# Performance work log

Hardware: AMD Instinct MI355X
Metric: run time of the kernel (lower is better)

The kernel has to match this reference:

```python
import jax, jax.numpy as jnp
import numpy as np

K = 3  # Chebyshev filter size (max_view)


def avwgcn(X, E, weights_pool, bias_pool):
    """Adaptive node-wise graph conv. X: [B,N,C_in], E: [N,D]."""
    N = E.shape[0]
    # adaptive adjacency: softmax over rows of relu(E E^T)
    supports = jax.nn.softmax(jax.nn.relu(E @ E.T), axis=1)  # [N,N]
    support_set = [jnp.eye(N, dtype=X.dtype), supports]
    for _ in range(2, K):  # Chebyshev recursion
        support_set.append(2.0 * supports @ support_set[-1] - support_set[-2])
    S = jnp.stack(support_set, axis=0)  # [K,N,N]
    W = jnp.einsum('nd,dkio->nkio', E, weights_pool)  # per-node weights [N,K,Ci,Co]
    bias = E @ bias_pool  # [N,Co]
    XG = jnp.einsum('knm,bmc->bnkc', S, X)  # [B,N,K,Ci]
    return jnp.einsum('bnki,nkio->bno', XG, W) + bias  # [B,N,Co]


def setup_inputs() -> dict:
    key = jax.random.key(0)
    ks = jax.random.split(key, 5)
    B, N, Cin, Cout, D = 32, 4096, 2, 64, 10
    Ci = Cin + Cout  # 66
    X = jax.random.normal(ks[0], (B, N, Cin), dtype=jnp.float32)
    H = jnp.zeros((B, N, Cout), dtype=jnp.float32)
    E = jax.random.normal(ks[1], (N, D), dtype=jnp.float32)
    W_gate = jax.random.normal(ks[2], (D, K, Ci, 2 * Cout), dtype=jnp.float32) * 0.1
    b_gate = jnp.zeros((D, 2 * Cout), dtype=jnp.float32)
    W_update = jax.random.normal(ks[3], (D, K, Ci, Cout), dtype=jnp.float32) * 0.1
    b_update = jnp.zeros((D, Cout), dtype=jnp.float32)
    return {"X": X, "H": H, "E": E, "W_gate": W_gate, "b_gate": b_gate,
            "W_update": W_update, "b_update": b_update}


def reference(X, H, E, W_gate, b_gate, W_update, b_update):
    Cout = H.shape[-1]
    XH = jnp.concatenate([X, H], axis=-1)  # [B,N,Cin+Cout]
    ZR = jax.nn.sigmoid(avwgcn(XH, E, W_gate, b_gate))  # [B,N,2*Cout]
    Z, R = ZR[..., :Cout], ZR[..., Cout:]
    C = jnp.concatenate([X, Z * H], axis=-1)
    HC = jnp.tanh(avwgcn(C, E, W_update, b_update))
    return R * H + (1.0 - R) * HC
```

## Files before the change

kernel.cpp:

```cpp
#include <hip/hip_runtime.h>
#include <math.h>

#define N_NODES 4096
#define BATCH   32
#define D_EMB   10
#define CIN     2
#define COUT    64
#define CI      66
#define KSUP    3
#define NCOLS   2112
#define NPAD    2176
#define LDT     4096

#define KSEC    72
#define KI_REAL 216
#define KILD    232
#define OCH     (32 * KILD)
#define WROW_G  (128 * KILD)
#define WROW_U  (64 * KILD)
#define WGT2_R  (WROW_G + WROW_U)

typedef _Float16 half_t;
typedef __attribute__((ext_vector_type(8))) _Float16 f16x8;
typedef __attribute__((ext_vector_type(4))) _Float16 f16x4;
typedef __attribute__((ext_vector_type(2))) _Float16 f16x2;
typedef __attribute__((ext_vector_type(4))) float f32x4;

union u32h2 { unsigned u; f16x2 h; };

struct __attribute__((packed, aligned(4))) uint4_u4 { uint4 v; };
__device__ __forceinline__ f16x8 loadu8h(const half_t* p) {
  union { uint4 u; f16x8 h; } r;
  r.u = ((const uint4_u4*)p)->v;
  return r.h;
}

__device__ __forceinline__ float fast_sigmoid(float x) { return 1.f / (1.f + __expf(-x)); }
__device__ __forceinline__ float fast_tanh(float x) { return 1.f - 2.f / (__expf(2.f * x) + 1.f); }

__device__ __forceinline__ void gld_lds16(const half_t* g, half_t* l) {
  __builtin_amdgcn_global_load_lds(
      (const __attribute__((address_space(1))) void*)g,
      (__attribute__((address_space(3))) void*)l, 16, 0, 0);
}

__global__ __launch_bounds__(256) void k_softmax_p(const float* __restrict__ E,
                                                   half_t* __restrict__ Pb) {
  const int n = blockIdx.x;
  const int tid = threadIdx.x;
  __shared__ float En[D_EMB];
  __shared__ float ms[256], ss[256];
  if (tid < D_EMB) En[tid] = E[n * D_EMB + tid];
  __syncthreads();
  float en[D_EMB];
#pragma unroll
  for (int d = 0; d < D_EMB; ++d) en[d] = En[d];

  float m = -1e30f, s = 0.f;
  for (int c = tid; c < N_NODES; c += 256) {
    const float* Ec = E + c * D_EMB;
    float v = 0.f;
#pragma unroll
    for (int d = 0; d < D_EMB; ++d) v += en[d] * Ec[d];
    v = fmaxf(v, 0.f);
    if (v > m) { s *= __expf(m - v); m = v; }
    s += __expf(v - m);
  }
  ms[tid] = m; ss[tid] = s;
  __syncthreads();
  for (int off = 128; off > 0; off >>= 1) {
    if (tid < off) {
      float m2 = ms[tid + off], s2 = ss[tid + off];
      float m1 = ms[tid], s1 = ss[tid];
      float mm = fmaxf(m1, m2);
      ms[tid] = mm;
      ss[tid] = s1 * __expf(m1 - mm) + s2 * __expf(m2 - mm);
    }
    __syncthreads();
  }
  const float M = ms[0];
  const float inv = 1.f / ss[0];
  half_t* Pr = Pb + (size_t)n * N_NODES;
  for (int c = tid; c < N_NODES; c += 256) {
    const float* Ec = E + c * D_EMB;
    float v = 0.f;
#pragma unroll
    for (int d = 0; d < D_EMB; ++d) v += en[d] * Ec[d];
    v = fmaxf(v, 0.f);
    Pr[c] = (half_t)(__expf(v - M) * inv);
  }
}

__global__ __launch_bounds__(256) void k_build_v0(const float* __restrict__ X,
                                                  const float* __restrict__ H,
                                                  half_t* __restrict__ Vt,
                                                  half_t* __restrict__ Vn,
                                                  half_t* __restrict__ Cbt,
                                                  half_t* __restrict__ Cbn) {
  size_t idx = (size_t)blockIdx.x * 256 + threadIdx.x;
  if (idx >= (size_t)N_NODES * NCOLS) return;
  const int m = (int)(idx / NCOLS);
  const int col = (int)(idx % NCOLS);
  const int b = col / CI;
  const int c = col % CI;
  float v;
  if (c < CIN) v = X[((size_t)b * N_NODES + m) * CIN + c];
  else         v = H[((size_t)b * N_NODES + m) * COUT + (c - CIN)];
  const half_t h = (half_t)v;
  Vn[(size_t)m * NPAD + col] = h;
  Vt[(size_t)col * LDT + m] = h;
  if (c < CIN) {
    Cbn[(size_t)m * NPAD + col] = h;
    Cbt[(size_t)col * LDT + m] = h;
  }
}

__device__ __forceinline__ void gemm_compute_tile(const half_t* __restrict__ Lb,
                                                  int wm, int wn, int fofs,
                                                  f32x4 (&acc)[4][4]) {
  const half_t* As_ = Lb;
  const half_t* Bs_ = Lb + 4096;
  f16x8 a[4], b[4];
#pragma unroll
  for (int i = 0; i < 4; ++i)
    a[i] = *(const f16x8*)&As_[((wm >> 4) + i) * 512 + fofs];
#pragma unroll
  for (int j = 0; j < 4; ++j)
    b[j] = *(const f16x8*)&Bs_[((wn >> 4) + j) * 512 + fofs];
  __builtin_amdgcn_s_setprio(1);
#pragma unroll
  for (int i = 0; i < 4; ++i)
#pragma unroll
    for (int j = 0; j < 4; ++j)
      acc[i][j] = __builtin_amdgcn_mfma_f32_16x16x32_f16(a[i], b[j], acc[i][j], 0, 0, 0);
  __builtin_amdgcn_s_setprio(0);
}

__global__ __launch_bounds__(256) void k_gemm_f16(const half_t* __restrict__ A,
                                                  const half_t* __restrict__ Bt,
                                                  half_t* __restrict__ Cn,
                                                  half_t* __restrict__ Ct) {
  __shared__ half_t LB[3][8192];
  const int tid = threadIdx.x;
  const int lane = tid & 63;
  const int wave = tid >> 6;

  int flat = blockIdx.y * 17 + blockIdx.x;
  flat = (flat & 7) * 68 + (flat >> 3);
  const int bx = flat % 17;
  const int by = flat / 17;

  const int wm = (wave >> 1) * 64;
  const int wn = (wave & 1) * 64;
  const int rb = by * 128;
  const int cb = bx * 128;

  const int srow = lane >> 2;
  const int skg = (((lane & 3) + ((lane >> 3) & 3)) & 3) * 8;
  const half_t* ga0 = A + (size_t)(rb + wave * 32 + srow) * N_NODES + skg;
  const half_t* ga1 = ga0 + (size_t)16 * N_NODES;
  const half_t* gb0 = Bt + (size_t)(cb + wave * 32 + srow) * LDT + skg;
  const half_t* gb1 = gb0 + (size_t)16 * LDT;
  const int lA0 = wave * 1024;
  const int lA1 = lA0 + 512;
  const int lB0 = 4096 + wave * 1024;
  const int lB1 = lB0 + 512;

  const int fr = lane & 15;
  const int fg = lane >> 4;
  const int fofs = (4 * fr + ((fg - (fr >> 1)) & 3)) * 8;

  f32x4 acc[4][4] = {};

#define STAGE_T(buf, kk) do { half_t* Lp = LB[(buf)]; \
    gld_lds16(ga0 + (kk), Lp + lA0); gld_lds16(ga1 + (kk), Lp + lA1); \
    gld_lds16(gb0 + (kk), Lp + lB0); gld_lds16(gb1 + (kk), Lp + lB1); } while (0)

  STAGE_T(0, 0);
  STAGE_T(1, 32);

  for (int t = 0; t < 126; t += 3) {
    asm volatile("s_waitcnt vmcnt(4)\n\ts_barrier" ::: "memory");
    STAGE_T(2, (t + 2) * 32);
    gemm_compute_tile(LB[0], wm, wn, fofs, acc);

    asm volatile("s_waitcnt vmcnt(4)\n\ts_barrier" ::: "memory");
    STAGE_T(0, (t + 3) * 32);
    gemm_compute_tile(LB[1], wm, wn, fofs, acc);

    asm volatile("s_waitcnt vmcnt(4)\n\ts_barrier" ::: "memory");
    STAGE_T(1, (t + 4) * 32);
    gemm_compute_tile(LB[2], wm, wn, fofs, acc);
  }
  asm volatile("s_waitcnt vmcnt(4)\n\ts_barrier" ::: "memory");
  gemm_compute_tile(LB[0], wm, wn, fofs, acc);
  asm volatile("s_waitcnt vmcnt(0)\n\ts_barrier" ::: "memory");
  gemm_compute_tile(LB[1], wm, wn, fofs, acc);
#undef STAGE_T

  const int en = lane & 15;
  const int em = (lane >> 4) * 4;
#pragma unroll
  for (int i = 0; i < 4; ++i) {
#pragma unroll
    for (int j = 0; j < 4; ++j) {
      const int m0 = rb + wm + i * 16 + em;
      const int n = cb + wn + j * 16 + en;
      half_t h0 = (half_t)acc[i][j][0];
      half_t h1 = (half_t)acc[i][j][1];
      half_t h2 = (half_t)acc[i][j][2];
      half_t h3 = (half_t)acc[i][j][3];
      if (Ct) {
        f16x4 t4 = {h0, h1, h2, h3};
        *(f16x4*)&Ct[(size_t)n * LDT + m0] = t4;
      }
      Cn[(size_t)(m0 + 0) * NPAD + n] = h0;
      Cn[(size_t)(m0 + 1) * NPAD + n] = h1;
      Cn[(size_t)(m0 + 2) * NPAD + n] = h2;
      Cn[(size_t)(m0 + 3) * NPAD + n] = h3;
    }
  }
}

__global__ __launch_bounds__(256) void k_wgt2(const float* __restrict__ Wg,
                                              const float* __restrict__ Wu,
                                              unsigned* __restrict__ WT2) {
  const int r = blockIdx.x * 256 + threadIdx.x;
  if (r >= WGT2_R) return;
  const float* pool;
  int o, ki, ostr;
  if (r < WROW_G) { o = r / KILD; ki = r % KILD; pool = Wg; ostr = 128; }
  else { int r2 = r - WROW_G; o = r2 / KILD; ki = r2 % KILD; pool = Wu; ostr = 64; }
  const int k = ki / KSEC;
  const int i = ki - k * KSEC;
#pragma unroll
  for (int dp = 0; dp < 5; ++dp) {
    u32h2 v; v.h = f16x2{(half_t)0.f, (half_t)0.f};
    if (ki < KI_REAL && i < CI) {
      v.h[0] = (half_t)pool[(((size_t)(2 * dp) * KSUP + k) * CI + i) * ostr + o];
      v.h[1] = (half_t)pool[(((size_t)(2 * dp + 1) * KSUP + k) * CI + i) * ostr + o];
    }
    WT2[(size_t)dp * WGT2_R + r] = v.u;
  }
}

__device__ __forceinline__ void stage_xg(const half_t* __restrict__ v0r,
                                         const half_t* __restrict__ g1r,
                                         const half_t* __restrict__ g2r,
                                         half_t* __restrict__ xg, int tid, int nthr) {
  for (int w = tid; w < 32 * 9; w += nthr) {
    const int b = w / 9;
    const int oct = w - b * 9;
    half_t* row = xg + b * KILD;
    const half_t* pv = v0r + b * CI;
    const half_t* pg1 = g1r + b * CI;
    const half_t* pg2 = g2r + b * CI;
    if (oct < 8) {
      const f16x8 v0 = loadu8h(pv + oct * 8);
      const f16x8 g1 = loadu8h(pg1 + oct * 8);
      const f16x8 g2 = loadu8h(pg2 + oct * 8);
      const f16x8 x2 = g2 + g2 - v0;
      *(f16x8*)&row[oct * 8] = v0;
      *(f16x8*)&row[KSEC + oct * 8] = g1;
      *(f16x8*)&row[2 * KSEC + oct * 8] = x2;
    } else {
      u32h2 tv, tg1, tg2;
      tv.u = *(const unsigned*)(pv + 64);
      tg1.u = *(const unsigned*)(pg1 + 64);
      tg2.u = *(const unsigned*)(pg2 + 64);
      f16x8 v0 = {}, g1 = {}, x2 = {};
      v0[0] = tv.h[0]; v0[1] = tv.h[1];
      g1[0] = tg1.h[0]; g1[1] = tg1.h[1];
      x2[0] = tg2.h[0] + tg2.h[0] - tv.h[0];
      x2[1] = tg2.h[1] + tg2.h[1] - tv.h[1];
      *(f16x8*)&row[64] = v0;
      *(f16x8*)&row[KSEC + 64] = g1;
      *(f16x8*)&row[2 * KSEC + 64] = x2;
    }
  }
  for (int w = tid; w < 32 * 2; w += nthr) {
    const f16x8 z = {};
    *(f16x8*)&xg[(w >> 1) * KILD + KI_REAL + (w & 1) * 8] = z;
  }
}

__global__ __launch_bounds__(512) void k_gate_t(const half_t* __restrict__ Vn,
                                                const half_t* __restrict__ G1n,
                                                const half_t* __restrict__ G2n,
                                                const unsigned* __restrict__ WT2,
                                                const float* __restrict__ E,
                                                const float* __restrict__ bg,
                                                const float* __restrict__ H,
                                                half_t* __restrict__ Cbn,
                                                half_t* __restrict__ Cbt,
                                                half_t* __restrict__ Rb) {
  const int n0 = blockIdx.x * 2;
  const int tid = threadIdx.x;
  const int lane = tid & 63;
  const int wave = tid >> 6;
  __shared__ half_t Wl[2][OCH];
  __shared__ half_t xg[2][OCH];
  __shared__ float biasl[2][128];

  f16x2 e2p0[5], e2p1[5];
#pragma unroll
  for (int dp = 0; dp < 5; ++dp) {
    e2p0[dp][0] = (half_t)E[n0 * D_EMB + 2 * dp];
    e2p0[dp][1] = (half_t)E[n0 * D_EMB + 2 * dp + 1];
    e2p1[dp][0] = (half_t)E[(n0 + 1) * D_EMB + 2 * dp];
    e2p1[dp][1] = (half_t)E[(n0 + 1) * D_EMB + 2 * dp + 1];
  }

  if (tid < 256) {
    const int nn = tid >> 7;
    const int o = tid & 127;
    float s = 0.f;
#pragma unroll
    for (int d = 0; d < D_EMB; ++d) s += E[(n0 + nn) * D_EMB + d] * bg[d * 128 + o];
    biasl[nn][o] = s;
  }
  stage_xg(Vn + (size_t)n0 * NPAD, G1n + (size_t)n0 * NPAD, G2n + (size_t)n0 * NPAD, xg[0], tid, 512);
  stage_xg(Vn + (size_t)(n0 + 1) * NPAD, G1n + (size_t)(n0 + 1) * NPAD, G2n + (size_t)(n0 + 1) * NPAD, xg[1], tid, 512);

  const int fr = lane & 15;
  const int fk = (lane >> 4) * 8;
  const int en = lane & 15;
  const int em = (lane >> 4) * 4;
  const int node = wave & 1;
  const int ot = (wave >> 1) & 1;
  const int bh = wave >> 2;
  const int nn = n0 + node;

#pragma unroll
  for (int p = 0; p < 4; ++p) {
    if (p > 0) __syncthreads();
    for (int base = tid * 8; base < OCH; base += 4096) {
      float a0[8] = {}, a1[8] = {};
#pragma unroll
      for (int dp = 0; dp < 5; ++dp) {
        const unsigned* wrow = WT2 + (size_t)dp * WGT2_R + p * OCH + base;
        uint4 wa = *(const uint4*)wrow;
        uint4 wb = *(const uint4*)(wrow + 4);
        u32h2 c0, c1, c2, c3;
        c0.u = wa.x; c1.u = wa.y; c2.u = wa.z; c3.u = wa.w;
        a0[0] = __builtin_amdgcn_fdot2(c0.h, e2p0[dp], a0[0], false);
        a0[1] = __builtin_amdgcn_fdot2(c1.h, e2p0[dp], a0[1], false);
        a0[2] = __builtin_amdgcn_fdot2(c2.h, e2p0[dp], a0[2], false);
        a0[3] = __builtin_amdgcn_fdot2(c3.h, e2p0[dp], a0[3], false);
        a1[0] = __builtin_amdgcn_fdot2(c0.h, e2p1[dp], a1[0], false);
        a1[1] = __builtin_amdgcn_fdot2(c1.h, e2p1[dp], a1[1], false);
        a1[2] = __builtin_amdgcn_fdot2(c2.h, e2p1[dp], a1[2], false);
        a1[3] = __builtin_amdgcn_fdot2(c3.h, e2p1[dp], a1[3], false);
        c0.u = wb.x; c1.u = wb.y; c2.u = wb.z; c3.u = wb.w;
        a0[4] = __builtin_amdgcn_fdot2(c0.h, e2p0[dp], a0[4], false);
        a0[5] = __builtin_amdgcn_fdot2(c1.h, e2p0[dp], a0[5], false);
        a0[6] = __builtin_amdgcn_fdot2(c2.h, e2p0[dp], a0[6], false);
        a0[7] = __builtin_amdgcn_fdot2(c3.h, e2p0[dp], a0[7], false);
        a1[4] = __builtin_amdgcn_fdot2(c0.h, e2p1[dp], a1[4], false);
        a1[5] = __builtin_amdgcn_fdot2(c1.h, e2p1[dp], a1[5], false);
        a1[6] = __builtin_amdgcn_fdot2(c2.h, e2p1[dp], a1[6], false);
        a1[7] = __builtin_amdgcn_fdot2(c3.h, e2p1[dp], a1[7], false);
      }
      f16x8 w0, w1;
#pragma unroll
      for (int e = 0; e < 8; ++e) { w0[e] = (half_t)a0[e]; w1[e] = (half_t)a1[e]; }
      *(f16x8*)&Wl[0][base] = w0;
      *(f16x8*)&Wl[1][base] = w1;
    }
    __syncthreads();

    f32x4 acc2 = {};
#pragma unroll
    for (int ks = 0; ks < 7; ++ks) {
      const f16x8 a0 = *(const f16x8*)&xg[node][(bh * 16 + fr) * KILD + ks * 32 + fk];
      const f16x8 b0 = *(const f16x8*)&Wl[node][(ot * 16 + fr) * KILD + ks * 32 + fk];
      acc2 = __builtin_amdgcn_mfma_f32_16x16x32_f16(a0, b0, acc2, 0, 0, 0);
    }
    const int o_g = p * 32 + ot * 16 + en;
    const float bo = biasl[node][o_g];
#pragma unroll
    for (int r = 0; r < 4; ++r) {
      const int b = bh * 16 + em + r;
      const float s = fast_sigmoid(acc2[r] + bo);
      if (p < 2) {
        const float hv = H[((size_t)b * N_NODES + nn) * COUT + o_g];
        const half_t z = (half_t)(s * hv);
        const int c0 = b * CI + CIN + o_g;
        Cbn[(size_t)nn * NPAD + c0] = z;
        Cbt[(size_t)c0 * LDT + nn] = z;
      } else {
        Rb[((size_t)b * N_NODES + nn) * COUT + (o_g - 64)] = (half_t)s;
      }
    }
  }
}

__global__ __launch_bounds__(512) void k_update_t(const half_t* __restrict__ Cbn,
                                                  const half_t* __restrict__ G1n,
                                                  const half_t* __restrict__ G2n,
                                                  const unsigned* __restrict__ WT2,
                                                  const float* __restrict__ E,
                                                  const float* __restrict__ bu,
                                                  const float* __restrict__ H,
                                                  const half_t* __restrict__ Rb,
                                                  float* __restrict__ Out) {
  const int n0 = blockIdx.x * 2;
  const int tid = threadIdx.x;
  const int lane = tid & 63;
  const int wave = tid >> 6;
  __shared__ half_t Wl[2][OCH];
  __shared__ half_t xg[2][OCH];
  __shared__ float biasl[2][64];

  f16x2 e2p0[5], e2p1[5];
#pragma unroll
  for (int dp = 0; dp < 5; ++dp) {
    e2p0[dp][0] = (half_t)E[n0 * D_EMB + 2 * dp];
    e2p0[dp][1] = (half_t)E[n0 * D_EMB + 2 * dp + 1];
    e2p1[dp][0] = (half_t)E[(n0 + 1) * D_EMB + 2 * dp];
    e2p1[dp][1] = (half_t)E[(n0 + 1) * D_EMB + 2 * dp + 1];
  }

  if (tid < 128) {
    const int nn = tid >> 6;
    const int o = tid & 63;
    float s = 0.f;
#pragma unroll
    for (int d = 0; d < D_EMB; ++d) s += E[(n0 + nn) * D_EMB + d] * bu[d * COUT + o];
    biasl[nn][o] = s;
  }
  stage_xg(Cbn + (size_t)n0 * NPAD, G1n + (size_t)n0 * NPAD, G2n + (size_t)n0 * NPAD, xg[0], tid, 512);
  stage_xg(Cbn + (size_t)(n0 + 1) * NPAD, G1n + (size_t)(n0 + 1) * NPAD, G2n + (size_t)(n0 + 1) * NPAD, xg[1], tid, 512);

  const int fr = lane & 15;
  const int fk = (lane >> 4) * 8;
  const int en = lane & 15;
  const int em = (lane >> 4) * 4;
  const int node = wave & 1;
  const int ot = (wave >> 1) & 1;
  const int bh = wave >> 2;
  const int nn = n0 + node;

#pragma unroll
  for (int p = 0; p < 2; ++p) {
    if (p > 0) __syncthreads();
    for (int base = tid * 8; base < OCH; base += 4096) {
      float a0[8] = {}, a1[8] = {};
#pragma unroll
      for (int dp = 0; dp < 5; ++dp) {
        const unsigned* wrow = WT2 + (size_t)dp * WGT2_R + WROW_G + p * OCH + base;
        uint4 wa = *(const uint4*)wrow;
        uint4 wb = *(const uint4*)(wrow + 4);
        u32h2 c0, c1, c2, c3;
        c0.u = wa.x; c1.u = wa.y; c2.u = wa.z; c3.u = wa.w;
        a0[0] = __builtin_amdgcn_fdot2(c0.h, e2p0[dp], a0[0], false);
        a0[1] = __builtin_amdgcn_fdot2(c1.h, e2p0[dp], a0[1], false);
        a0[2] = __builtin_amdgcn_fdot2(c2.h, e2p0[dp], a0[2], false);
        a0[3] = __builtin_amdgcn_fdot2(c3.h, e2p0[dp], a0[3], false);
        a1[0] = __builtin_amdgcn_fdot2(c0.h, e2p1[dp], a1[0], false);
        a1[1] = __builtin_amdgcn_fdot2(c1.h, e2p1[dp], a1[1], false);
        a1[2] = __builtin_amdgcn_fdot2(c2.h, e2p1[dp], a1[2], false);
        a1[3] = __builtin_amdgcn_fdot2(c3.h, e2p1[dp], a1[3], false);
        c0.u = wb.x; c1.u = wb.y; c2.u = wb.z; c3.u = wb.w;
        a0[4] = __builtin_amdgcn_fdot2(c0.h, e2p0[dp], a0[4], false);
        a0[5] = __builtin_amdgcn_fdot2(c1.h, e2p0[dp], a0[5], false);
        a0[6] = __builtin_amdgcn_fdot2(c2.h, e2p0[dp], a0[6], false);
        a0[7] = __builtin_amdgcn_fdot2(c3.h, e2p0[dp], a0[7], false);
        a1[4] = __builtin_amdgcn_fdot2(c0.h, e2p1[dp], a1[4], false);
        a1[5] = __builtin_amdgcn_fdot2(c1.h, e2p1[dp], a1[5], false);
        a1[6] = __builtin_amdgcn_fdot2(c2.h, e2p1[dp], a1[6], false);
        a1[7] = __builtin_amdgcn_fdot2(c3.h, e2p1[dp], a1[7], false);
      }
      f16x8 w0, w1;
#pragma unroll
      for (int e = 0; e < 8; ++e) { w0[e] = (half_t)a0[e]; w1[e] = (half_t)a1[e]; }
      *(f16x8*)&Wl[0][base] = w0;
      *(f16x8*)&Wl[1][base] = w1;
    }
    __syncthreads();

    f32x4 acc2 = {};
#pragma unroll
    for (int ks = 0; ks < 7; ++ks) {
      const f16x8 a0 = *(const f16x8*)&xg[node][(bh * 16 + fr) * KILD + ks * 32 + fk];
      const f16x8 b0 = *(const f16x8*)&Wl[node][(ot * 16 + fr) * KILD + ks * 32 + fk];
      acc2 = __builtin_amdgcn_mfma_f32_16x16x32_f16(a0, b0, acc2, 0, 0, 0);
    }
    const int o = p * 32 + ot * 16 + en;
    const float bo = biasl[node][o];
#pragma unroll
    for (int r = 0; r < 4; ++r) {
      const int b = bh * 16 + em + r;
      const float hc = fast_tanh(acc2[r] + bo);
      const size_t base = ((size_t)b * N_NODES + nn) * COUT + o;
      const float hv = H[base];
      const float rr = (float)Rb[base];
      Out[base] = rr * hv + (1.f - rr) * hc;
    }
  }
}

extern "C" void kernel_launch(void* const* d_in, const int* in_sizes, int n_in,
                              void* d_out, int out_size, void* d_ws, size_t ws_size,
                              hipStream_t stream) {
  const float* X  = (const float*)d_in[0];
  const float* H  = (const float*)d_in[1];
  const float* E  = (const float*)d_in[2];
  const float* Wg = (const float*)d_in[3];
  const float* bg = (const float*)d_in[4];
  const float* Wu = (const float*)d_in[5];
  const float* bu = (const float*)d_in[6];
  float* out = (float*)d_out;

  const size_t SZ_P = (size_t)N_NODES * N_NODES;
  const size_t SZ_M = (size_t)NPAD * LDT;
  half_t* Pb  = (half_t*)d_ws;
  half_t* Vt  = Pb + SZ_P;
  half_t* Vn  = Vt + SZ_M;
  half_t* G1t = Vn + SZ_M;
  half_t* G1n = G1t + SZ_M;
  half_t* G2n = G1n + SZ_M;
  half_t* Cbt = G2n + SZ_M;
  half_t* Cbn = Cbt + SZ_M;
  half_t* Rb  = Cbn + SZ_M;
  unsigned* WT2 = (unsigned*)(Rb + (size_t)BATCH * N_NODES * COUT);

  k_softmax_p<<<N_NODES, 256, 0, stream>>>(E, Pb);
  {
    const size_t tot = (size_t)N_NODES * NCOLS;
    k_build_v0<<<(int)((tot + 255) / 256), 256, 0, stream>>>(X, H, Vt, Vn, Cbt, Cbn);
  }
  k_wgt2<<<(WGT2_R + 255) / 256, 256, 0, stream>>>(Wg, Wu, WT2);

  dim3 gg(NPAD / 128, N_NODES / 128);
  k_gemm_f16<<<gg, 256, 0, stream>>>(Pb, Vt, G1n, G1t);
  k_gemm_f16<<<gg, 256, 0, stream>>>(Pb, G1t, G2n, nullptr);
  k_gate_t<<<N_NODES / 2, 512, 0, stream>>>(Vn, G1n, G2n, WT2, E, bg, H, Cbn, Cbt, Rb);
  k_gemm_f16<<<gg, 256, 0, stream>>>(Pb, Cbt, G1n, G1t);
  k_gemm_f16<<<gg, 256, 0, stream>>>(Pb, G1t, G2n, nullptr);
  k_update_t<<<N_NODES / 2, 512, 0, stream>>>(Cbn, G1n, G2n, WT2, E, bu, H, Rb, out);
}
```

Measured before the change: 790.9 us.

## Split-K the propagation GEMMs into two halves with a separate reduction kernel

Each of the four N×N by N×2176 propagation GEMMs now runs as two K-halves (grid 17×32×2, 1088 blocks instead of 544), writing fp32 partials to workspace. A new reduction kernel sums the halves, casts to fp16 and writes both the normal and transposed outputs. The aim is to fill more compute units than the original 544-block grid, at the cost of writing and re-reading two fp32 partial buffers of about 35 MB each per GEMM, plus four extra launches. The old path is kept as a fallback when the workspace is too small.

Result: slower. 812.1 us (+2.7%).

```diff
diff --git a/kernel.cpp b/kernel.cpp
--- a/kernel.cpp
+++ b/kernel.cpp
@@ -136,6 +136,132 @@
   __builtin_amdgcn_s_setprio(0);
 }
 
+__global__ __launch_bounds__(256) void k_gemm_ks(const half_t* __restrict__ A,
+                                                 const half_t* __restrict__ Bt,
+                                                 float* __restrict__ Pw) {
+  __shared__ half_t LB[3][8192];
+  const int tid = threadIdx.x;
+  const int lane = tid & 63;
+  const int wave = tid >> 6;
+
+  int flat = blockIdx.z * 544 + blockIdx.y * 17 + blockIdx.x;
+  flat = (flat & 7) * 136 + (flat >> 3);
+  const int h = flat / 544;
+  const int rem = flat - h * 544;
+  const int bx = rem % 17;
+  const int by = rem / 17;
+  const int k0 = h * 2048;
+
+  const int wm = (wave >> 1) * 64;
+  const int wn = (wave & 1) * 64;
+  const int rb = by * 128;
+  const int cb = bx * 128;
+
+  const int srow = lane >> 2;
+  const int skg = (((lane & 3) + ((lane >> 3) & 3)) & 3) * 8;
+  const half_t* ga0 = A + (size_t)(rb + wave * 32 + srow) * N_NODES + k0 + skg;
+  const half_t* ga1 = ga0 + (size_t)16 * N_NODES;
+  const half_t* gb0 = Bt + (size_t)(cb + wave * 32 + srow) * LDT + k0 + skg;
+  const half_t* gb1 = gb0 + (size_t)16 * LDT;
+  const int lA0 = wave * 1024;
+  const int lA1 = lA0 + 512;
+  const int lB0 = 4096 + wave * 1024;
+  const int lB1 = lB0 + 512;
+
+  const int fr = lane & 15;
+  const int fg = lane >> 4;
+  const int fofs = (4 * fr + ((fg - (fr >> 1)) & 3)) * 8;
+
+  f32x4 acc[4][4] = {};
+
+#define STAGE_K(buf, kk) do { half_t* Lp = LB[(buf)]; \
+    gld_lds16(ga0 + (kk), Lp + lA0); gld_lds16(ga1 + (kk), Lp + lA1); \
+    gld_lds16(gb0 + (kk), Lp + lB0); gld_lds16(gb1 + (kk), Lp + lB1); } while (0)
+
+  STAGE_K(0, 0);
+  STAGE_K(1, 32);
+  for (int t = 0; t < 60; t += 3) {
+    asm volatile("s_waitcnt vmcnt(4)\n\ts_barrier" ::: "memory");
+    STAGE_K(2, (t + 2) * 32);
+    gemm_compute_tile(LB[0], wm, wn, fofs, acc);
+
+    asm volatile("s_waitcnt vmcnt(4)\n\ts_barrier" ::: "memory");
+    STAGE_K(0, (t + 3) * 32);
+    gemm_compute_tile(LB[1], wm, wn, fofs, acc);
+
+    asm volatile("s_waitcnt vmcnt(4)\n\ts_barrier" ::: "memory");
+    STAGE_K(1, (t + 4) * 32);
+    gemm_compute_tile(LB[2], wm, wn, fofs, acc);
+  }
+  asm volatile("s_waitcnt vmcnt(4)\n\ts_barrier" ::: "memory");
+  STAGE_K(2, 62 * 32);
+  gemm_compute_tile(LB[0], wm, wn, fofs, acc);
+  asm volatile("s_waitcnt vmcnt(4)\n\ts_barrier" ::: "memory");
+  STAGE_K(0, 63 * 32);
+  gemm_compute_tile(LB[1], wm, wn, fofs, acc);
+  asm volatile("s_waitcnt vmcnt(4)\n\ts_barrier" ::: "memory");
+  gemm_compute_tile(LB[2], wm, wn, fofs, acc);
+  asm volatile("s_waitcnt vmcnt(0)\n\ts_barrier" ::: "memory");
+  gemm_compute_tile(LB[0], wm, wn, fofs, acc);
+#undef STAGE_K
+
+  float* Pq = Pw + (size_t)h * ((size_t)N_NODES * NPAD);
+  const int en = lane & 15;
+  const int em = (lane >> 4) * 4;
+#pragma unroll
+  for (int i = 0; i < 4; ++i) {
+#pragma unroll
+    for (int j = 0; j < 4; ++j) {
+      const int m0 = rb + wm + i * 16 + em;
+      const int n = cb + wn + j * 16 + en;
+      Pq[(size_t)(m0 + 0) * NPAD + n] = acc[i][j][0];
+      Pq[(size_t)(m0 + 1) * NPAD + n] = acc[i][j][1];
+      Pq[(size_t)(m0 + 2) * NPAD + n] = acc[i][j][2];
+      Pq[(size_t)(m0 + 3) * NPAD + n] = acc[i][j][3];
+    }
+  }
+}
+
+__global__ __launch_bounds__(256) void k_red(const float* __restrict__ P0,
+                                             const float* __restrict__ P1,
+                                             half_t* __restrict__ Cn,
+                                             half_t* __restrict__ Ct) {
+  __shared__ half_t T[64][69];
+  const int tid = threadIdx.x;
+  const int nb = blockIdx.x * 64;
+  const int mb = blockIdx.y * 64;
+  const int c4 = (tid & 15) * 4;
+  const int r0 = tid >> 4;
+#pragma unroll
+  for (int it = 0; it < 4; ++it) {
+    const int r = r0 + it * 16;
+    const size_t off = (size_t)(mb + r) * NPAD + nb + c4;
+    const float4 a = *(const float4*)&P0[off];
+    const float4 b = *(const float4*)&P1[off];
+    const half_t v0 = (half_t)(a.x + b.x);
+    const half_t v1 = (half_t)(a.y + b.y);
+    const half_t v2 = (half_t)(a.z + b.z);
+    const half_t v3 = (half_t)(a.w + b.w);
+    f16x4 v = {v0, v1, v2, v3};
+    *(f16x4*)&Cn[off] = v;
+    if (Ct) {
+      T[r][c4 + 0] = v0;
+      T[r][c4 + 1] = v1;
+      T[r][c4 + 2] = v2;
+      T[r][c4 + 3] = v3;
+    }
+  }
+  if (!Ct) return;
+  __syncthreads();
+#pragma unroll
+  for (int it = 0; it < 4; ++it) {
+    const int n2 = r0 + it * 16;
+    const int m4 = c4;
+    f16x4 v = {T[m4 + 0][n2], T[m4 + 1][n2], T[m4 + 2][n2], T[m4 + 3][n2]};
+    *(f16x4*)&Ct[(size_t)(nb + n2) * LDT + mb + m4] = v;
+  }
+}
+
 __global__ __launch_bounds__(256) void k_gemm_f16(const half_t* __restrict__ A,
                                                   const half_t* __restrict__ Bt,
                                                   half_t* __restrict__ Cn,
@@ -178,7 +304,6 @@
 
   STAGE_T(0, 0);
   STAGE_T(1, 32);
-
   for (int t = 0; t < 126; t += 3) {
     asm volatile("s_waitcnt vmcnt(4)\n\ts_barrier" ::: "memory");
     STAGE_T(2, (t + 2) * 32);
@@ -525,6 +650,12 @@
   half_t* Rb  = Cbn + SZ_M;
   unsigned* WT2 = (unsigned*)(Rb + (size_t)BATCH * N_NODES * COUT);
 
+  const size_t SZC = (size_t)N_NODES * NPAD;
+  size_t wt2_end = (size_t)((char*)(WT2 + 5 * (size_t)WGT2_R) - (char*)d_ws);
+  size_t pofs = (wt2_end + 255) & ~(size_t)255;
+  const bool split = ws_size >= pofs + 2 * SZC * sizeof(float);
+  float* Pw = (float*)((char*)d_ws + pofs);
+
   k_softmax_p<<<N_NODES, 256, 0, stream>>>(E, Pb);
   {
     const size_t tot = (size_t)N_NODES * NCOLS;
@@ -532,11 +663,29 @@
   }
   k_wgt2<<<(WGT2_R + 255) / 256, 256, 0, stream>>>(Wg, Wu, WT2);
 
-  dim3 gg(NPAD / 128, N_NODES / 128);
-  k_gemm_f16<<<gg, 256, 0, stream>>>(Pb, Vt, G1n, G1t);
-  k_gemm_f16<<<gg, 256, 0, stream>>>(Pb, G1t, G2n, nullptr);
+  const dim3 gk(17, 32, 2);
+  const dim3 gr(34, 64);
+  const dim3 gg(17, 32);
+
+  if (split) {
+    k_gemm_ks<<<gk, 256, 0, stream>>>(Pb, Vt, Pw);
+    k_red<<<gr, 256, 0, stream>>>(Pw, Pw + SZC, G1n, G1t);
+    k_gemm_ks<<<gk, 256, 0, stream>>>(Pb, G1t, Pw);
+    k_red<<<gr, 256, 0, stream>>>(Pw, Pw + SZC, G2n, nullptr);
+  } else {
+    k_gemm_f16<<<gg, 256, 0, stream>>>(Pb, Vt, G1n, G1t);
+    k_gemm_f16<<<gg, 256, 0, stream>>>(Pb, G1t, G2n, nullptr);
+  }
   k_gate_t<<<N_NODES / 2, 512, 0, stream>>>(Vn, G1n, G2n, WT2, E, bg, H, Cbn, Cbt, Rb);
-  k_gemm_f16<<<gg, 256, 0, stream>>>(Pb, Cbt, G1n, G1t);
-  k_gemm_f16<<<gg, 256, 0, stream>>>(Pb, G1t, G2n, nullptr);
+
+  if (split) {
+    k_gemm_ks<<<gk, 256, 0, stream>>>(Pb, Cbt, Pw);
+    k_red<<<gr, 256, 0, stream>>>(Pw, Pw + SZC, G1n, G1t);
+    k_gemm_ks<<<gk, 256, 0, stream>>>(Pb, G1t, Pw);
+    k_red<<<gr, 256, 0, stream>>>(Pw, Pw + SZC, G2n, nullptr);
+  } else {
+    k_gemm_f16<<<gg, 256, 0, stream>>>(Pb, Cbt, G1n, G1t);
+    k_gemm_f16<<<gg, 256, 0, stream>>>(Pb, G1t, G2n, nullptr);
+  }
   k_update_t<<<N_NODES / 2, 512, 0, stream>>>(Cbn, G1n, G2n, WT2, E, bu, H, Rb, out);
 }
```

## Replace scattered transposed stores with a tiled LDS transpose kernel

Applied to the files above, without the earlier changes.

The gate kernel and the build kernel stop writing the transposed copy Cbt with strided per-element stores. Instead a new k_tr kernel transposes Cbn into Cbt through a shared-memory tile, giving coalesced reads and writes. The Rb buffer layout also changes to node-major, so the gate and update kernels access it contiguously. This adds one kernel launch and an extra full read/write pass over the buffer in exchange for removing the uncoalesced scatter.

After: 762.2 us. 3.6% less time.

```diff
diff --git a/kernel.cpp b/kernel.cpp
--- a/kernel.cpp
+++ b/kernel.cpp
@@ -95,7 +95,6 @@
                                                   const float* __restrict__ H,
                                                   half_t* __restrict__ Vt,
                                                   half_t* __restrict__ Vn,
-                                                  half_t* __restrict__ Cbt,
                                                   half_t* __restrict__ Cbn) {
   size_t idx = (size_t)blockIdx.x * 256 + threadIdx.x;
   if (idx >= (size_t)N_NODES * NCOLS) return;
@@ -109,10 +108,7 @@
   const half_t h = (half_t)v;
   Vn[(size_t)m * NPAD + col] = h;
   Vt[(size_t)col * LDT + m] = h;
-  if (c < CIN) {
-    Cbn[(size_t)m * NPAD + col] = h;
-    Cbt[(size_t)col * LDT + m] = h;
-  }
+  if (c < CIN) Cbn[(size_t)m * NPAD + col] = h;
 }
 
 __device__ __forceinline__ void gemm_compute_tile(const half_t* __restrict__ Lb,
@@ -178,7 +174,6 @@
 
   STAGE_T(0, 0);
   STAGE_T(1, 32);
-
   for (int t = 0; t < 126; t += 3) {
     asm volatile("s_waitcnt vmcnt(4)\n\ts_barrier" ::: "memory");
     STAGE_T(2, (t + 2) * 32);
@@ -219,6 +214,33 @@
       Cn[(size_t)(m0 + 2) * NPAD + n] = h2;
       Cn[(size_t)(m0 + 3) * NPAD + n] = h3;
     }
+  }
+}
+
+__global__ __launch_bounds__(256) void k_tr(const half_t* __restrict__ Cbn,
+                                            half_t* __restrict__ Ct) {
+  __shared__ half_t T[64][69];
+  const int tid = threadIdx.x;
+  const int cb = blockIdx.x * 64;
+  const int mb = blockIdx.y * 64;
+  const int c4 = (tid & 15) * 4;
+  const int r0 = tid >> 4;
+#pragma unroll
+  for (int it = 0; it < 4; ++it) {
+    const int r = r0 + it * 16;
+    f16x4 v = *(const f16x4*)&Cbn[(size_t)(mb + r) * NPAD + cb + c4];
+    T[r][c4 + 0] = v[0];
+    T[r][c4 + 1] = v[1];
+    T[r][c4 + 2] = v[2];
+    T[r][c4 + 3] = v[3];
+  }
+  __syncthreads();
+#pragma unroll
+  for (int it = 0; it < 4; ++it) {
+    const int c2 = r0 + it * 16;
+    const int m4 = c4;
+    f16x4 v = {T[m4 + 0][c2], T[m4 + 1][c2], T[m4 + 2][c2], T[m4 + 3][c2]};
+    *(f16x4*)&Ct[(size_t)(cb + c2) * LDT + mb + m4] = v;
   }
 }
 
@@ -292,7 +314,6 @@
                                                 const float* __restrict__ bg,
                                                 const float* __restrict__ H,
                                                 half_t* __restrict__ Cbn,
-                                                half_t* __restrict__ Cbt,
                                                 half_t* __restrict__ Rb) {
   const int n0 = blockIdx.x * 2;
   const int tid = threadIdx.x;
@@ -385,11 +406,9 @@
       if (p < 2) {
         const float hv = H[((size_t)b * N_NODES + nn) * COUT + o_g];
         const half_t z = (half_t)(s * hv);
-        const int c0 = b * CI + CIN + o_g;
-        Cbn[(size_t)nn * NPAD + c0] = z;
-        Cbt[(size_t)c0 * LDT + nn] = z;
+        Cbn[(size_t)nn * NPAD + b * CI + CIN + o_g] = z;
       } else {
-        Rb[((size_t)b * N_NODES + nn) * COUT + (o_g - 64)] = (half_t)s;
+        Rb[(size_t)nn * 2048 + b * COUT + (o_g - 64)] = (half_t)s;
       }
     }
   }
@@ -492,10 +511,9 @@
     for (int r = 0; r < 4; ++r) {
       const int b = bh * 16 + em + r;
       const float hc = fast_tanh(acc2[r] + bo);
-      const size_t base = ((size_t)b * N_NODES + nn) * COUT + o;
-      const float hv = H[base];
-      const float rr = (float)Rb[base];
-      Out[base] = rr * hv + (1.f - rr) * hc;
+      const float hv = H[((size_t)b * N_NODES + nn) * COUT + o];
+      const float rr = (float)Rb[(size_t)nn * 2048 + b * COUT + o];
+      Out[((size_t)b * N_NODES + nn) * COUT + o] = rr * hv + (1.f - rr) * hc;
     }
   }
 }
@@ -528,14 +546,18 @@
   k_softmax_p<<<N_NODES, 256, 0, stream>>>(E, Pb);
   {
     const size_t tot = (size_t)N_NODES * NCOLS;
-    k_build_v0<<<(int)((tot + 255) / 256), 256, 0, stream>>>(X, H, Vt, Vn, Cbt, Cbn);
+    k_build_v0<<<(int)((tot + 255) / 256), 256, 0, stream>>>(X, H, Vt, Vn, Cbn);
   }
   k_wgt2<<<(WGT2_R + 255) / 256, 256, 0, stream>>>(Wg, Wu, WT2);
 
-  dim3 gg(NPAD / 128, N_NODES / 128);
+  const dim3 gg(17, 32);
+  const dim3 gt(33, 64);
+
   k_gemm_f16<<<gg, 256, 0, stream>>>(Pb, Vt, G1n, G1t);
   k_gemm_f16<<<gg, 256, 0, stream>>>(Pb, G1t, G2n, nullptr);
-  k_gate_t<<<N_NODES / 2, 512, 0, stream>>>(Vn, G1n, G2n, WT2, E, bg, H, Cbn, Cbt, Rb);
+  k_gate_t<<<N_NODES / 2, 512, 0, stream>>>(Vn, G1n, G2n, WT2, E, bg, H, Cbn, Rb);
+  k_tr<<<gt, 256, 0, stream>>>(Cbn, Cbt);
+
   k_gemm_f16<<<gg, 256, 0, stream>>>(Pb, Cbt, G1n, G1t);
   k_gemm_f16<<<gg, 256, 0, stream>>>(Pb, G1t, G2n, nullptr);
   k_update_t<<<N_NODES / 2, 512, 0, stream>>>(Cbn, G1n, G2n, WT2, E, bu, H, Rb, out);
```
